# Optimization experiments

Measured on AMD Instinct MI355X. Metric: run time of the kernel, lower is better.

## Reference

```python
import jax, jax.numpy as jnp
import numpy as np

N, FIN, NH, NR, F, E = 50000, 256, 4, 4, 64, 500000


def setup_inputs() -> dict:
    key = jax.random.key(0)
    ks = jax.random.split(key, 12)
    x = jax.random.normal(ks[0], (N, FIN), jnp.float32)
    src = jax.random.randint(ks[1], (E,), 0, N)
    trg = jax.random.randint(ks[2], (E,), 0, N)
    rel = jax.random.randint(ks[3], (E,), 0, NR)
    node_to_graph_map = jnp.zeros((N,), jnp.int32)
    s = 1.0 / np.sqrt(FIN)
    W_proj = jax.random.uniform(ks[4], (NH * NR * F, FIN), jnp.float32, -s, s)
    score_src = jax.random.normal(ks[5], (1, NH, NR, F), jnp.float32) * 0.1
    score_trg = jax.random.normal(ks[6], (1, NH, NR, F), jnp.float32) * 0.1
    sf = 1.0 / np.sqrt(F)
    W1 = jax.random.uniform(ks[7], (F, F), jnp.float32, -sf, sf)
    b1 = jnp.zeros((F,), jnp.float32)
    W2 = jax.random.uniform(ks[8], (F, F), jnp.float32, -sf, sf)
    b2 = jnp.zeros((F,), jnp.float32)
    W3 = jax.random.uniform(ks[9], (1, F), jnp.float32, -sf, sf)
    b3 = jnp.zeros((1,), jnp.float32)
    W_skip = jax.random.uniform(ks[10], (NH * F, FIN), jnp.float32, -s, s)
    bias = jnp.zeros((NH * F,), jnp.float32)
    gamma = jnp.ones((NH * F,), jnp.float32)
    beta = jnp.zeros((NH * F,), jnp.float32)
    return dict(x=x, src=src, trg=trg, rel=rel, node_to_graph_map=node_to_graph_map,
                W_proj=W_proj, score_src=score_src, score_trg=score_trg,
                W1=W1, b1=b1, W2=W2, b2=b2, W3=W3, b3=b3,
                W_skip=W_skip, bias=bias, gamma=gamma, beta=beta)


def mish(v):
    return v * jnp.tanh(jax.nn.softplus(v))


def gat_forward(x, W_proj, score_src, score_trg, W1, b1, W2, b2, W3, b3,
                W_skip, bias, gamma, beta, src, trg, rel):
    n = x.shape[0]
    # (N, NH, NR, F) projected node features
    proj = (x @ W_proj.T).reshape(n, NH, NR, F)
    s_src = (proj * score_src).sum(-1)  # (N, NH, NR)
    s_trg = (proj * score_trg).sum(-1)  # (N, NH, NR)
    # lift to edges for their own relation: (E, NH)
    e_s = s_src[src, :, rel] + s_trg[trg, :, rel]
    e_s = jax.nn.leaky_relu(e_s, 0.2)
    # per-(relation, head) max over edges (matches per-relation max(dim=0) in the torch loop)
    m = jax.ops.segment_max(e_s, rel, num_segments=NR)  # (NR, NH)
    e_exp = jnp.exp(e_s - m[rel])
    # segment softmax grouped by (target node, relation)
    seg = trg * NR + rel
    denom = jax.ops.segment_sum(e_exp, seg, num_segments=n * NR)  # (N*NR, NH)
    att = e_exp / (denom[seg] + 1e-16)  # (E, NH)
    feat = proj[src, :, rel, :] * att[:, :, None]  # (E, NH, F)
    agg = jax.ops.segment_sum(feat, seg, num_segments=n * NR)  # (N*NR, NH, F)
    agg = agg.reshape(n, NR, NH, F).transpose(0, 2, 1, 3)  # (N, NH, NR, F)
    # AttentionedAggregationLayer: MLP score -> Mish -> softmax over relation dim -> weighted sum
    h = jax.nn.relu(agg @ W1.T + b1)
    h = jax.nn.relu(h @ W2.T + b2)
    sc = mish(h @ W3.T + b3)            # (N, NH, NR, 1)
    a_rel = jax.nn.softmax(sc, axis=-2)
    out = (agg * a_rel).sum(-2)          # (N, NH, F)
    # skip connection (FIN != NH*F per-head, so projected skip), concat heads, bias, ELU, LayerNorm
    out = out + (x @ W_skip.T).reshape(n, NH, F)
    out = out.reshape(n, NH * F) + bias
    out = jax.nn.elu(out)
    mu = out.mean(-1, keepdims=True)
    var = out.var(-1, keepdims=True)
    out = (out - mu) * jax.lax.rsqrt(var + 1e-5) * gamma + beta
    return out


def reference(x, src, trg, rel, node_to_graph_map, W_proj, score_src, score_trg,
              W1, b1, W2, b2, W3, b3, W_skip, bias, gamma, beta):
    return gat_forward(x, W_proj, score_src, score_trg, W1, b1, W2, b2, W3, b3,
                       W_skip, bias, gamma, beta, src, trg, rel)
```

## Files before the change

kernel.cpp:

```cpp
#include <hip/hip_runtime.h>

#define NNODES 50000
#define NEDGES 500000
#define NBINS  (NNODES * 4)
#define NSCANB 196
#define MPAD   50176

#define WF_W1    0
#define WF_B1    4096
#define WF_W2    4160
#define WF_B2    8256
#define WF_W3    8320
#define WF_B3    8384
#define WF_SSC   8388
#define WF_STC   9412
#define WF_BIAS  10436
#define WF_GAMMA 10692
#define WF_BETA  10948
#define WF_TOT   11204

typedef __attribute__((ext_vector_type(8))) short short8;
typedef __attribute__((ext_vector_type(4))) short short4v;
typedef __attribute__((ext_vector_type(4))) float floatx4;
typedef __attribute__((ext_vector_type(4))) unsigned int uint4v;

__device__ __forceinline__ float bf2f(unsigned short u) {
    return __uint_as_float(((unsigned)u) << 16);
}
__device__ __forceinline__ unsigned f2bf(float f) {
    unsigned u = __float_as_uint(f);
    u += 0x7fffu + ((u >> 16) & 1u);
    return u >> 16;
}
__device__ __forceinline__ int clampi(int v, int hi) { return v < 0 ? 0 : (v > hi ? hi : v); }

__device__ __forceinline__ short8 pack_bf16(const float* p) {
    short8 r;
#pragma unroll
    for (int j = 0; j < 8; j++) r[j] = (short)f2bf(p[j]);
    return r;
}

__global__ __launch_bounds__(256) void probe_k(const unsigned short* __restrict__ xs,
                                               unsigned* __restrict__ flag) {
    __shared__ unsigned cnt;
    if (threadIdx.x == 0) cnt = 0;
    __syncthreads();
    unsigned local = 0;
    for (int i = threadIdx.x; i < 8192; i += 256) {
        float v = bf2f(xs[i]);
        if (!(fabsf(v) < 1e10f)) local++;
    }
    atomicAdd(&cnt, local);
    __syncthreads();
    if (threadIdx.x == 0) *flag = (cnt > 256u) ? 1u : 0u;
}

__device__ __forceinline__ float ldf(const void* p, int i, bool f32) {
    return f32 ? ((const float*)p)[i] : bf2f(((const unsigned short*)p)[i]);
}

__global__ __launch_bounds__(1024) void wconv_k(const void* W1, const void* b1,
                                                const void* W2, const void* b2,
                                                const void* W3, const void* b3,
                                                const void* ssc, const void* stc,
                                                const void* bias, const void* gamma,
                                                const void* beta,
                                                const unsigned* __restrict__ flag,
                                                float* __restrict__ wf) {
    bool f32 = (*flag != 0u);
    for (int i = threadIdx.x; i < WF_TOT; i += 1024) {
        float v;
        if (i < WF_B1)          v = ldf(W1, i - WF_W1, f32);
        else if (i < WF_W2)     v = ldf(b1, i - WF_B1, f32);
        else if (i < WF_B2)     v = ldf(W2, i - WF_W2, f32);
        else if (i < WF_W3)     v = ldf(b2, i - WF_B2, f32);
        else if (i < WF_B3)     v = ldf(W3, i - WF_W3, f32);
        else if (i < WF_SSC) {
            int j = i - WF_B3;
            v = (j < 1) ? ldf(b3, j, f32) : 0.f;
        }
        else if (i < WF_STC)    v = ldf(ssc, i - WF_SSC, f32);
        else if (i < WF_BIAS)   v = ldf(stc, i - WF_STC, f32);
        else if (i < WF_GAMMA)  v = ldf(bias, i - WF_BIAS, f32);
        else if (i < WF_BETA)   v = ldf(gamma, i - WF_GAMMA, f32);
        else                    v = ldf(beta, i - WF_BETA, f32);
        wf[i] = v;
    }
}

__global__ __launch_bounds__(256) void convbf_k(const void* __restrict__ src,
                                                unsigned short* __restrict__ dst,
                                                int nelem, int npad,
                                                const unsigned* __restrict__ flag) {
    int i8 = (blockIdx.x * 256 + threadIdx.x) * 8;
    if (i8 >= npad) return;
    short8 o;
    if (i8 < nelem) {
        if (*flag) {
            const float* pf = (const float*)src + i8;
            floatx4 a = *(const floatx4*)pf;
            floatx4 b = *(const floatx4*)(pf + 4);
            o[0] = (short)f2bf(a[0]); o[1] = (short)f2bf(a[1]);
            o[2] = (short)f2bf(a[2]); o[3] = (short)f2bf(a[3]);
            o[4] = (short)f2bf(b[0]); o[5] = (short)f2bf(b[1]);
            o[6] = (short)f2bf(b[2]); o[7] = (short)f2bf(b[3]);
        } else {
            o = *(const short8*)((const unsigned short*)src + i8);
        }
    } else {
#pragma unroll
        for (int j = 0; j < 8; j++) o[j] = 0;
    }
    *(short8*)(dst + i8) = o;
}

__global__ __launch_bounds__(64) void gemm_fused_k(const unsigned short* __restrict__ A,
                                                   const unsigned short* __restrict__ Bp,
                                                   const unsigned short* __restrict__ Bs,
                                                   unsigned short* __restrict__ proj,
                                                   unsigned short* __restrict__ out16,
                                                   float* __restrict__ out32,
                                                   const float* __restrict__ wf,
                                                   float* __restrict__ s_src,
                                                   float* __restrict__ s_trg,
                                                   const unsigned* __restrict__ flag) {
    const bool cf32 = (*flag != 0u);
    const int lane = threadIdx.x & 63;
    const int l15 = lane & 15, q = lane >> 4;
    const int m0 = blockIdx.x * 64;
    const int cg0 = blockIdx.y * 4;

    short8 af[4][8];
#pragma unroll
    for (int mt = 0; mt < 4; mt++)
#pragma unroll
        for (int ks = 0; ks < 8; ks++)
            af[mt][ks] = *(const short8*)(A + (size_t)(m0 + mt * 16 + l15) * 256 + ks * 32 + q * 8);

    if (cg0 < 16) {
#pragma unroll 1
        for (int cgi = 0; cgi < 4; cgi++) {
            const int cg = cg0 + cgi;
            floatx4 acc[4][4];
#pragma unroll
            for (int i = 0; i < 4; i++)
#pragma unroll
                for (int j = 0; j < 4; j++) acc[i][j] = (floatx4){0.f, 0.f, 0.f, 0.f};
#pragma unroll
            for (int ks = 0; ks < 8; ks++) {
                short8 bfr[4];
#pragma unroll
                for (int nt = 0; nt < 4; nt++)
                    bfr[nt] = *(const short8*)(Bp + (size_t)(cg * 64 + nt * 16 + l15) * 256 + ks * 32 + q * 8);
#pragma unroll
                for (int mt = 0; mt < 4; mt++)
#pragma unroll
                    for (int nt = 0; nt < 4; nt++)
                        acc[mt][nt] = __builtin_amdgcn_mfma_f32_16x16x32_bf16(bfr[nt], af[mt][ks],
                                                                             acc[mt][nt], 0, 0, 0);
            }
            const int h = cg >> 2, r = cg & 3;
            const int colbase = (r * 4 + h) * 64;
            const int cell = r * 4 + h;
            const int scell = h * 4 + r;
            floatx4 sa4[4], sb4[4];
#pragma unroll
            for (int nt = 0; nt < 4; nt++) {
                sa4[nt] = *(const floatx4*)(wf + WF_SSC + scell * 64 + nt * 16 + q * 4);
                sb4[nt] = *(const floatx4*)(wf + WF_STC + scell * 64 + nt * 16 + q * 4);
            }
#pragma unroll
            for (int mt = 0; mt < 4; mt++) {
                const int row = m0 + mt * 16 + l15;
                float pa = 0.f, pb = 0.f;
#pragma unroll
                for (int nt = 0; nt < 4; nt++) {
                    short4v sv;
#pragma unroll
                    for (int rg = 0; rg < 4; rg++) {
                        float v = acc[mt][nt][rg];
                        unsigned short vb = (unsigned short)f2bf(v);
                        sv[rg] = (short)vb;
                        float vr = bf2f(vb);
                        pa = fmaf(vr, sa4[nt][rg], pa);
                        pb = fmaf(vr, sb4[nt][rg], pb);
                    }
                    if (row < NNODES)
                        *(short4v*)(proj + (size_t)row * 1024 + colbase + nt * 16 + q * 4) = sv;
                }
                pa += __shfl_xor(pa, 16);
                pa += __shfl_xor(pa, 32);
                pb += __shfl_xor(pb, 16);
                pb += __shfl_xor(pb, 32);
                if (q == 0 && row < NNODES) {
                    s_src[row * 16 + cell] = pa;
                    s_trg[row * 16 + cell] = pb;
                }
            }
        }
    } else {
#pragma unroll 1
        for (int cg = 0; cg < 4; cg++) {
            floatx4 acc[4][4];
#pragma unroll
            for (int i = 0; i < 4; i++)
#pragma unroll
                for (int j = 0; j < 4; j++) acc[i][j] = (floatx4){0.f, 0.f, 0.f, 0.f};
#pragma unroll
            for (int ks = 0; ks < 8; ks++) {
                short8 bfr[4];
#pragma unroll
                for (int nt = 0; nt < 4; nt++)
                    bfr[nt] = *(const short8*)(Bs + (size_t)(cg * 64 + nt * 16 + l15) * 256 + ks * 32 + q * 8);
#pragma unroll
                for (int mt = 0; mt < 4; mt++)
#pragma unroll
                    for (int nt = 0; nt < 4; nt++)
                        acc[mt][nt] = __builtin_amdgcn_mfma_f32_16x16x32_bf16(bfr[nt], af[mt][ks],
                                                                             acc[mt][nt], 0, 0, 0);
            }
#pragma unroll
            for (int mt = 0; mt < 4; mt++) {
                const int row = m0 + mt * 16 + l15;
                if (row >= NNODES) continue;
#pragma unroll
                for (int nt = 0; nt < 4; nt++) {
                    if (cf32) {
                        floatx4 o = acc[mt][nt];
                        *(floatx4*)(out32 + (size_t)row * 256 + cg * 64 + nt * 16 + q * 4) = o;
                    } else {
                        short4v sv;
#pragma unroll
                        for (int rg = 0; rg < 4; rg++)
                            sv[rg] = (short)f2bf(acc[mt][nt][rg]);
                        *(short4v*)(out16 + (size_t)row * 256 + cg * 64 + nt * 16 + q * 4) = sv;
                    }
                }
            }
        }
    }
}

__global__ __launch_bounds__(256) void count_k(const int* __restrict__ trg,
                                               const int* __restrict__ rel,
                                               unsigned* __restrict__ counts, int E) {
    int e = blockIdx.x * 256 + threadIdx.x;
    if (e >= E) return;
    int g = clampi(trg[e], NNODES - 1);
    int r = clampi(rel[e], 3);
    atomicAdd(&counts[g * 4 + r], 1u);
}

__global__ __launch_bounds__(256) void scan1_k(const unsigned* __restrict__ counts,
                                               unsigned* __restrict__ offsets,
                                               unsigned* __restrict__ bsum) {
    __shared__ unsigned ts[256];
    int t = threadIdx.x;
    int base = blockIdx.x * 1024 + t * 4;
    uint4v c = {0u, 0u, 0u, 0u};
    if (base + 3 < NBINS) c = *(const uint4v*)(counts + base);
    else {
#pragma unroll
        for (int j = 0; j < 4; j++) c[j] = (base + j < NBINS) ? counts[base + j] : 0u;
    }
    ts[t] = c[0] + c[1] + c[2] + c[3];
    __syncthreads();
    for (int off = 1; off < 256; off <<= 1) {
        unsigned v = (t >= off) ? ts[t - off] : 0u;
        __syncthreads();
        ts[t] += v;
        __syncthreads();
    }
    unsigned pre = (t == 0) ? 0u : ts[t - 1];
    uint4v o;
    o[0] = pre;
    o[1] = pre + c[0];
    o[2] = pre + c[0] + c[1];
    o[3] = pre + c[0] + c[1] + c[2];
    if (base + 3 < NBINS) *(uint4v*)(offsets + base) = o;
    else {
#pragma unroll
        for (int j = 0; j < 4; j++) if (base + j < NBINS) offsets[base + j] = o[j];
    }
    if (t == 255) bsum[blockIdx.x] = ts[255];
}

__global__ __launch_bounds__(256) void scan2_k(unsigned* __restrict__ bsum,
                                               unsigned* __restrict__ offsets) {
    __shared__ unsigned ts[256];
    int t = threadIdx.x;
    unsigned v = (t < NSCANB) ? bsum[t] : 0u;
    ts[t] = v;
    __syncthreads();
    for (int off = 1; off < 256; off <<= 1) {
        unsigned u = (t >= off) ? ts[t - off] : 0u;
        __syncthreads();
        ts[t] += u;
        __syncthreads();
    }
    if (t < NSCANB) bsum[t] = (t == 0) ? 0u : ts[t - 1];
    if (t == 255) offsets[NBINS] = ts[255];
}

__global__ __launch_bounds__(256) void scan3_k(unsigned* __restrict__ offsets,
                                               unsigned* __restrict__ cursor,
                                               const unsigned* __restrict__ bsum) {
    int t = threadIdx.x;
    unsigned base = bsum[blockIdx.x];
    int idx = blockIdx.x * 1024 + t * 4;
    if (idx + 3 < NBINS) {
        uint4v o = *(const uint4v*)(offsets + idx);
        o[0] += base; o[1] += base; o[2] += base; o[3] += base;
        *(uint4v*)(offsets + idx) = o;
        *(uint4v*)(cursor + idx) = o;
    } else {
#pragma unroll
        for (int j = 0; j < 4; j++)
            if (idx + j < NBINS) {
                unsigned v = offsets[idx + j] + base;
                offsets[idx + j] = v;
                cursor[idx + j] = v;
            }
    }
}

__global__ __launch_bounds__(256) void fill_k(const int* __restrict__ src,
                                              const int* __restrict__ trg,
                                              const int* __restrict__ rel,
                                              const float* __restrict__ s_src,
                                              const float* __restrict__ s_trg,
                                              unsigned* __restrict__ cursor,
                                              unsigned* __restrict__ esrc,
                                              floatx4* __restrict__ eexp, int E) {
    int e = blockIdx.x * 256 + threadIdx.x;
    if (e >= E) return;
    int s = clampi(src[e], NNODES - 1);
    int g = clampi(trg[e], NNODES - 1);
    int r = clampi(rel[e], 3);
    unsigned pos = atomicAdd(&cursor[g * 4 + r], 1u);
    if (pos >= (unsigned)E) pos = E - 1;
    esrc[pos] = (unsigned)s;
    floatx4 aa = *(const floatx4*)(s_src + s * 16 + r * 4);
    floatx4 bb = *(const floatx4*)(s_trg + g * 16 + r * 4);
    floatx4 v;
#pragma unroll
    for (int h = 0; h < 4; h++) {
        float val = aa[h] + bb[h];
        val = val > 0.f ? val : 0.2f * val;
        v[h] = expf(val);
    }
    eexp[pos] = v;
}

__global__ __launch_bounds__(256) void rowagg2_k(const unsigned* __restrict__ offsets,
                                                 const unsigned* __restrict__ esrc,
                                                 const floatx4* __restrict__ eexp,
                                                 const unsigned short* __restrict__ proj,
                                                 unsigned short* __restrict__ agg) {
    int wave = threadIdx.x >> 6, lane = threadIdx.x & 63;
    int bin = blockIdx.x * 4 + wave;
    if (bin >= NBINS) return;
    int r = bin & 3;
    int h = lane >> 4;
    unsigned beg = offsets[bin], end = offsets[bin + 1];

    float a0 = 0.f, a1 = 0.f, a2 = 0.f, a3 = 0.f, den = 0.f;
    unsigned i = beg;
    for (; i + 2 <= end; i += 2) {
        unsigned s0 = esrc[i], s1 = esrc[i + 1];
        floatx4 pe0 = eexp[i], pe1 = eexp[i + 1];
        short4v v0 = *((const short4v*)(proj + (size_t)s0 * 1024 + r * 256) + lane);
        short4v v1 = *((const short4v*)(proj + (size_t)s1 * 1024 + r * 256) + lane);
        float p0 = pe0[h], p1 = pe1[h];
        den += p0 + p1;
        a0 = fmaf(p0, bf2f((unsigned short)v0[0]), a0);
        a1 = fmaf(p0, bf2f((unsigned short)v0[1]), a1);
        a2 = fmaf(p0, bf2f((unsigned short)v0[2]), a2);
        a3 = fmaf(p0, bf2f((unsigned short)v0[3]), a3);
        a0 = fmaf(p1, bf2f((unsigned short)v1[0]), a0);
        a1 = fmaf(p1, bf2f((unsigned short)v1[1]), a1);
        a2 = fmaf(p1, bf2f((unsigned short)v1[2]), a2);
        a3 = fmaf(p1, bf2f((unsigned short)v1[3]), a3);
    }
    if (i < end) {
        unsigned s0 = esrc[i];
        floatx4 pe0 = eexp[i];
        short4v v0 = *((const short4v*)(proj + (size_t)s0 * 1024 + r * 256) + lane);
        float p0 = pe0[h];
        den += p0;
        a0 = fmaf(p0, bf2f((unsigned short)v0[0]), a0);
        a1 = fmaf(p0, bf2f((unsigned short)v0[1]), a1);
        a2 = fmaf(p0, bf2f((unsigned short)v0[2]), a2);
        a3 = fmaf(p0, bf2f((unsigned short)v0[3]), a3);
    }
    float inv = 1.f / (den + 1e-16f);
    short4v o;
    o[0] = (short)f2bf(a0 * inv);
    o[1] = (short)f2bf(a1 * inv);
    o[2] = (short)f2bf(a2 * inv);
    o[3] = (short)f2bf(a3 * inv);
    *((short4v*)(agg + (size_t)bin * 256) + lane) = o;
}

__global__ __launch_bounds__(256, 2) void mlp_mfma_k(const unsigned short* __restrict__ agg,
                                                     const float* __restrict__ wf,
                                                     float* __restrict__ sc) {
    __shared__ float lds[4][16 * 68];
    const int wave = threadIdx.x >> 6;
    const int lane = threadIdx.x & 63;
    const int l15 = lane & 15, q = lane >> 4;
    float* L = lds[wave];

    short8 w1f[2][4], w2f[2][4];
#pragma unroll
    for (int ks = 0; ks < 2; ks++)
#pragma unroll
        for (int nt = 0; nt < 4; nt++) {
            w1f[ks][nt] = pack_bf16(wf + WF_W1 + (nt * 16 + l15) * 64 + ks * 32 + q * 8);
            w2f[ks][nt] = pack_bf16(wf + WF_W2 + (nt * 16 + l15) * 64 + ks * 32 + q * 8);
        }
    float b1v[4], b2v[4], w3v[4];
#pragma unroll
    for (int nt = 0; nt < 4; nt++) {
        b1v[nt] = wf[WF_B1 + nt * 16 + l15];
        b2v[nt] = wf[WF_B2 + nt * 16 + l15];
        w3v[nt] = wf[WF_W3 + nt * 16 + l15];
    }
    float b3v = wf[WF_B3];

    int wave_id = blockIdx.x * 4 + wave;
#pragma unroll 1
    for (int t = 0; t < 4; t++) {
        int row0 = (wave_id * 4 + t) * 16;
        short8 a1[2];
#pragma unroll
        for (int ks = 0; ks < 2; ks++)
            a1[ks] = *(const short8*)(agg + (size_t)(row0 + l15) * 64 + ks * 32 + q * 8);
        floatx4 acc1[4];
#pragma unroll
        for (int nt = 0; nt < 4; nt++) {
            acc1[nt] = (floatx4){0.f, 0.f, 0.f, 0.f};
            acc1[nt] = __builtin_amdgcn_mfma_f32_16x16x32_bf16(a1[0], w1f[0][nt], acc1[nt], 0, 0, 0);
            acc1[nt] = __builtin_amdgcn_mfma_f32_16x16x32_bf16(a1[1], w1f[1][nt], acc1[nt], 0, 0, 0);
        }
#pragma unroll
        for (int nt = 0; nt < 4; nt++)
#pragma unroll
            for (int rg = 0; rg < 4; rg++)
                L[(q * 4 + rg) * 68 + nt * 16 + l15] = fmaxf(acc1[nt][rg] + b1v[nt], 0.f);
        short8 a2[2];
#pragma unroll
        for (int ks = 0; ks < 2; ks++) {
            short8 rr;
#pragma unroll
            for (int j = 0; j < 8; j++)
                rr[j] = (short)f2bf(L[l15 * 68 + ks * 32 + q * 8 + j]);
            a2[ks] = rr;
        }
        floatx4 acc2[4];
#pragma unroll
        for (int nt = 0; nt < 4; nt++) {
            acc2[nt] = (floatx4){0.f, 0.f, 0.f, 0.f};
            acc2[nt] = __builtin_amdgcn_mfma_f32_16x16x32_bf16(a2[0], w2f[0][nt], acc2[nt], 0, 0, 0);
            acc2[nt] = __builtin_amdgcn_mfma_f32_16x16x32_bf16(a2[1], w2f[1][nt], acc2[nt], 0, 0, 0);
        }
        float p[4];
#pragma unroll
        for (int rg = 0; rg < 4; rg++) {
            float s = 0.f;
#pragma unroll
            for (int nt = 0; nt < 4; nt++)
                s = fmaf(fmaxf(acc2[nt][rg] + b2v[nt], 0.f), w3v[nt], s);
            p[rg] = s;
        }
#pragma unroll
        for (int off = 1; off < 16; off <<= 1) {
#pragma unroll
            for (int rg = 0; rg < 4; rg++) p[rg] += __shfl_xor(p[rg], off);
        }
        if (l15 == 0) {
#pragma unroll
            for (int rg = 0; rg < 4; rg++) {
                float acc = p[rg] + b3v;
                float sp = fmaxf(acc, 0.f) + log1pf(expf(-fabsf(acc)));
                float m = acc * tanhf(sp);
                int s_id = row0 + q * 4 + rg;
                int n = s_id >> 4, r = (s_id >> 2) & 3, h = s_id & 3;
                sc[n * 16 + h * 4 + r] = m;
            }
        }
    }
}

__global__ __launch_bounds__(256) void final_k(const unsigned short* __restrict__ agg,
                                               const float* __restrict__ sc,
                                               const float* __restrict__ wf,
                                               const unsigned* __restrict__ flag,
                                               unsigned short* __restrict__ out16,
                                               float* __restrict__ out32) {
    const bool f32 = (*flag != 0u);
    const int wave = threadIdx.x >> 6, lane = threadIdx.x & 63;
    const int n = blockIdx.x * 4 + wave;
    const int h = lane >> 4;
    const int c0 = h * 64 + (lane & 15) * 4;

    floatx4 sv = *(const floatx4*)(sc + n * 16 + h * 4);
    float mx = fmaxf(fmaxf(sv[0], sv[1]), fmaxf(sv[2], sv[3]));
    float e0 = expf(sv[0] - mx), e1 = expf(sv[1] - mx);
    float e2 = expf(sv[2] - mx), e3 = expf(sv[3] - mx);
    float inv = 1.f / (e0 + e1 + e2 + e3);
    float er[4] = {e0 * inv, e1 * inv, e2 * inv, e3 * inv};

    float acc4[4] = {0.f, 0.f, 0.f, 0.f};
#pragma unroll
    for (int r = 0; r < 4; r++) {
        short4v av = *(const short4v*)(agg + (size_t)n * 1024 + r * 256 + c0);
        float e = er[r];
        acc4[0] = fmaf(e, bf2f((unsigned short)av[0]), acc4[0]);
        acc4[1] = fmaf(e, bf2f((unsigned short)av[1]), acc4[1]);
        acc4[2] = fmaf(e, bf2f((unsigned short)av[2]), acc4[2]);
        acc4[3] = fmaf(e, bf2f((unsigned short)av[3]), acc4[3]);
    }

    const size_t ob = (size_t)n * 256 + c0;
    float v[4];
    floatx4 bi = *(const floatx4*)(wf + WF_BIAS + c0);
    if (f32) {
        floatx4 sk = *(const floatx4*)(out32 + ob);
#pragma unroll
        for (int j = 0; j < 4; j++) v[j] = acc4[j] + sk[j] + bi[j];
    } else {
        short4v sk = *(const short4v*)(out16 + ob);
#pragma unroll
        for (int j = 0; j < 4; j++) v[j] = acc4[j] + bf2f((unsigned short)sk[j]) + bi[j];
    }
#pragma unroll
    for (int j = 0; j < 4; j++) v[j] = v[j] > 0.f ? v[j] : expm1f(v[j]);

    float s = v[0] + v[1] + v[2] + v[3];
    float qq = v[0] * v[0] + v[1] * v[1] + v[2] * v[2] + v[3] * v[3];
#pragma unroll
    for (int o = 1; o < 64; o <<= 1) {
        s += __shfl_xor(s, o);
        qq += __shfl_xor(qq, o);
    }
    float mu = s * (1.f / 256.f);
    float var = fmaxf(qq * (1.f / 256.f) - mu * mu, 0.f);
    float rstd = rsqrtf(var + 1e-5f);

    floatx4 ga = *(const floatx4*)(wf + WF_GAMMA + c0);
    floatx4 be = *(const floatx4*)(wf + WF_BETA + c0);
    if (f32) {
        floatx4 o4;
#pragma unroll
        for (int j = 0; j < 4; j++) o4[j] = (v[j] - mu) * rstd * ga[j] + be[j];
        *(floatx4*)(out32 + ob) = o4;
    } else {
        short4v o4;
#pragma unroll
        for (int j = 0; j < 4; j++) o4[j] = (short)f2bf((v[j] - mu) * rstd * ga[j] + be[j]);
        *(short4v*)(out16 + ob) = o4;
    }
}

extern "C" void kernel_launch(void* const* d_in, const int* in_sizes, int n_in,
                              void* d_out, int out_size, void* d_ws, size_t ws_size,
                              hipStream_t stream) {
    if (ws_size < 226900000) return;

    const void* x      = d_in[0];
    const int* src     = (const int*)d_in[1];
    const int* trg     = (const int*)d_in[2];
    const int* rel     = (const int*)d_in[3];
    const void* W_proj = d_in[5];
    const void* ssc    = d_in[6];
    const void* stc    = d_in[7];
    const void* W1     = d_in[8];
    const void* b1     = d_in[9];
    const void* W2     = d_in[10];
    const void* b2     = d_in[11];
    const void* W3     = d_in[12];
    const void* b3     = d_in[13];
    const void* W_skip = d_in[14];
    const void* bias   = d_in[15];
    const void* gamma  = d_in[16];
    const void* beta   = d_in[17];
    unsigned short* out16 = (unsigned short*)d_out;
    float* out32          = (float*)d_out;

    char* w = (char*)d_ws;
    unsigned short* proj = (unsigned short*)(w + 0);
    unsigned short* agg  = (unsigned short*)(w + 102400000);
    unsigned short* xbf  = (unsigned short*)(w + 102400000);
    float* s_src         = (float*)(w + 204800000);
    float* s_trg         = (float*)(w + 208000000);
    floatx4* eexp        = (floatx4*)(w + 211200000);
    unsigned short* wpbf = (unsigned short*)(w + 211200000);
    unsigned short* wsbf = (unsigned short*)(w + 212300000);
    unsigned* esrc       = (unsigned*)(w + 219200000);
    unsigned* counts     = (unsigned*)(w + 221200000);
    unsigned* offsets    = (unsigned*)(w + 222000000);
    unsigned* cursor     = (unsigned*)(w + 222800016);
    float* sc            = (float*)(w + 223600016);
    float* wf            = (float*)(w + 226800016);
    unsigned* flag       = (unsigned*)(w + 226844840);
    unsigned* bsum       = (unsigned*)(w + 226844848);

    hipMemsetAsync(counts, 0, NBINS * 4, stream);

    probe_k<<<1, 256, 0, stream>>>((const unsigned short*)x, flag);
    wconv_k<<<1, 1024, 0, stream>>>(W1, b1, W2, b2, W3, b3, ssc, stc, bias, gamma, beta,
                                    flag, wf);
    convbf_k<<<(MPAD * 256) / (8 * 256), 256, 0, stream>>>(x, xbf, NNODES * 256,
                                                           MPAD * 256, flag);
    convbf_k<<<128, 256, 0, stream>>>(W_proj, wpbf, 1024 * 256, 1024 * 256, flag);
    convbf_k<<<32, 256, 0, stream>>>(W_skip, wsbf, 256 * 256, 256 * 256, flag);
    gemm_fused_k<<<dim3(784, 5), 64, 0, stream>>>(xbf, wpbf, wsbf, proj, out16, out32,
                                                  wf, s_src, s_trg, flag);
    count_k<<<1954, 256, 0, stream>>>(trg, rel, counts, NEDGES);
    scan1_k<<<NSCANB, 256, 0, stream>>>(counts, offsets, bsum);
    scan2_k<<<1, 256, 0, stream>>>(bsum, offsets);
    scan3_k<<<NSCANB, 256, 0, stream>>>(offsets, cursor, bsum);
    fill_k<<<1954, 256, 0, stream>>>(src, trg, rel, s_src, s_trg, cursor, esrc, eexp, NEDGES);
    rowagg2_k<<<NBINS / 4, 256, 0, stream>>>(offsets, esrc, eexp, proj, agg);
    mlp_mfma_k<<<3125, 256, 0, stream>>>(agg, wf, sc);
    final_k<<<12500, 256, 0, stream>>>(agg, sc, wf, flag, out16, out32);
}
```

Measured before the change: 532.8 us.

## Fuse edge aggregation, relation MLP and final LayerNorm into one per-node kernel

Merges the row aggregation, MFMA MLP scoring and final softmax/skip/ELU/LayerNorm kernels into one kernel. Each wave handles whole nodes and keeps the aggregated features in LDS, so the agg and score buffers never go through global memory. MLP weights are converted to bf16 once in the weight conversion kernel instead of in every wave. The cost is fewer independent waves for the irregular gather (3125 blocks, each wave walking 4 nodes serially) and more LDS per block, which may reduce latency hiding for the gather.

```diff
diff --git a/kernel.cpp b/kernel.cpp
--- a/kernel.cpp
+++ b/kernel.cpp
@@ -18,6 +18,7 @@
 #define WF_GAMMA 10692
 #define WF_BETA  10948
 #define WF_TOT   11204
+#define WB_TOT   8192
 
 typedef __attribute__((ext_vector_type(8))) short short8;
 typedef __attribute__((ext_vector_type(4))) short short4v;
@@ -33,13 +34,6 @@
     return u >> 16;
 }
 __device__ __forceinline__ int clampi(int v, int hi) { return v < 0 ? 0 : (v > hi ? hi : v); }
-
-__device__ __forceinline__ short8 pack_bf16(const float* p) {
-    short8 r;
-#pragma unroll
-    for (int j = 0; j < 8; j++) r[j] = (short)f2bf(p[j]);
-    return r;
-}
 
 __global__ __launch_bounds__(256) void probe_k(const unsigned short* __restrict__ xs,
                                                unsigned* __restrict__ flag) {
@@ -67,9 +61,16 @@
                                                 const void* bias, const void* gamma,
                                                 const void* beta,
                                                 const unsigned* __restrict__ flag,
-                                                float* __restrict__ wf) {
+                                                float* __restrict__ wf,
+                                                unsigned short* __restrict__ wbf16) {
     bool f32 = (*flag != 0u);
-    for (int i = threadIdx.x; i < WF_TOT; i += 1024) {
+    for (int i = threadIdx.x; i < WF_TOT + WB_TOT; i += 1024) {
+        if (i >= WF_TOT) {
+            int j = i - WF_TOT;
+            float v = (j < 4096) ? ldf(W1, j, f32) : ldf(W2, j - 4096, f32);
+            wbf16[j] = (unsigned short)f2bf(v);
+            continue;
+        }
         float v;
         if (i < WF_B1)          v = ldf(W1, i - WF_W1, f32);
         else if (i < WF_W2)     v = ldf(b1, i - WF_B1, f32);
@@ -353,19 +354,10 @@
     eexp[pos] = v;
 }
 
-__global__ __launch_bounds__(256) void rowagg2_k(const unsigned* __restrict__ offsets,
-                                                 const unsigned* __restrict__ esrc,
-                                                 const floatx4* __restrict__ eexp,
-                                                 const unsigned short* __restrict__ proj,
-                                                 unsigned short* __restrict__ agg) {
-    int wave = threadIdx.x >> 6, lane = threadIdx.x & 63;
-    int bin = blockIdx.x * 4 + wave;
-    if (bin >= NBINS) return;
-    int r = bin & 3;
-    int h = lane >> 4;
-    unsigned beg = offsets[bin], end = offsets[bin + 1];
-
-    float a0 = 0.f, a1 = 0.f, a2 = 0.f, a3 = 0.f, den = 0.f;
+__device__ __forceinline__ void edge_acc(const unsigned* esrc, const floatx4* eexp,
+                                         const unsigned short* proj, int r, int h,
+                                         int lane, unsigned beg, unsigned end,
+                                         float* a, float* den) {
     unsigned i = beg;
     for (; i + 2 <= end; i += 2) {
         unsigned s0 = esrc[i], s1 = esrc[i + 1];
@@ -373,52 +365,54 @@
         short4v v0 = *((const short4v*)(proj + (size_t)s0 * 1024 + r * 256) + lane);
         short4v v1 = *((const short4v*)(proj + (size_t)s1 * 1024 + r * 256) + lane);
         float p0 = pe0[h], p1 = pe1[h];
-        den += p0 + p1;
-        a0 = fmaf(p0, bf2f((unsigned short)v0[0]), a0);
-        a1 = fmaf(p0, bf2f((unsigned short)v0[1]), a1);
-        a2 = fmaf(p0, bf2f((unsigned short)v0[2]), a2);
-        a3 = fmaf(p0, bf2f((unsigned short)v0[3]), a3);
-        a0 = fmaf(p1, bf2f((unsigned short)v1[0]), a0);
-        a1 = fmaf(p1, bf2f((unsigned short)v1[1]), a1);
-        a2 = fmaf(p1, bf2f((unsigned short)v1[2]), a2);
-        a3 = fmaf(p1, bf2f((unsigned short)v1[3]), a3);
+        *den += p0 + p1;
+        a[0] = fmaf(p0, bf2f((unsigned short)v0[0]), a[0]);
+        a[1] = fmaf(p0, bf2f((unsigned short)v0[1]), a[1]);
+        a[2] = fmaf(p0, bf2f((unsigned short)v0[2]), a[2]);
+        a[3] = fmaf(p0, bf2f((unsigned short)v0[3]), a[3]);
+        a[0] = fmaf(p1, bf2f((unsigned short)v1[0]), a[0]);
+        a[1] = fmaf(p1, bf2f((unsigned short)v1[1]), a[1]);
+        a[2] = fmaf(p1, bf2f((unsigned short)v1[2]), a[2]);
+        a[3] = fmaf(p1, bf2f((unsigned short)v1[3]), a[3]);
     }
     if (i < end) {
         unsigned s0 = esrc[i];
         floatx4 pe0 = eexp[i];
         short4v v0 = *((const short4v*)(proj + (size_t)s0 * 1024 + r * 256) + lane);
         float p0 = pe0[h];
-        den += p0;
-        a0 = fmaf(p0, bf2f((unsigned short)v0[0]), a0);
-        a1 = fmaf(p0, bf2f((unsigned short)v0[1]), a1);
-        a2 = fmaf(p0, bf2f((unsigned short)v0[2]), a2);
-        a3 = fmaf(p0, bf2f((unsigned short)v0[3]), a3);
-    }
-    float inv = 1.f / (den + 1e-16f);
-    short4v o;
-    o[0] = (short)f2bf(a0 * inv);
-    o[1] = (short)f2bf(a1 * inv);
-    o[2] = (short)f2bf(a2 * inv);
-    o[3] = (short)f2bf(a3 * inv);
-    *((short4v*)(agg + (size_t)bin * 256) + lane) = o;
-}
-
-__global__ __launch_bounds__(256, 2) void mlp_mfma_k(const unsigned short* __restrict__ agg,
-                                                     const float* __restrict__ wf,
-                                                     float* __restrict__ sc) {
-    __shared__ float lds[4][16 * 68];
+        *den += p0;
+        a[0] = fmaf(p0, bf2f((unsigned short)v0[0]), a[0]);
+        a[1] = fmaf(p0, bf2f((unsigned short)v0[1]), a[1]);
+        a[2] = fmaf(p0, bf2f((unsigned short)v0[2]), a[2]);
+        a[3] = fmaf(p0, bf2f((unsigned short)v0[3]), a[3]);
+    }
+}
+
+__global__ __launch_bounds__(256) void node_fused_k(const unsigned* __restrict__ offsets,
+                                                    const unsigned* __restrict__ esrc,
+                                                    const floatx4* __restrict__ eexp,
+                                                    const unsigned short* __restrict__ proj,
+                                                    const unsigned short* __restrict__ wbf16,
+                                                    const float* __restrict__ wf,
+                                                    const unsigned* __restrict__ flag,
+                                                    unsigned short* __restrict__ out16,
+                                                    float* __restrict__ out32) {
+    __shared__ unsigned short aggL[4][16 * 72];
+    __shared__ float hidL[4][16 * 68];
+    const bool f32 = (*flag != 0u);
     const int wave = threadIdx.x >> 6;
     const int lane = threadIdx.x & 63;
     const int l15 = lane & 15, q = lane >> 4;
-    float* L = lds[wave];
+    unsigned short* aL = aggL[wave];
+    float* hL = hidL[wave];
 
     short8 w1f[2][4], w2f[2][4];
 #pragma unroll
     for (int ks = 0; ks < 2; ks++)
 #pragma unroll
         for (int nt = 0; nt < 4; nt++) {
-            w1f[ks][nt] = pack_bf16(wf + WF_W1 + (nt * 16 + l15) * 64 + ks * 32 + q * 8);
-            w2f[ks][nt] = pack_bf16(wf + WF_W2 + (nt * 16 + l15) * 64 + ks * 32 + q * 8);
+            w1f[ks][nt] = *(const short8*)(wbf16 + (nt * 16 + l15) * 64 + ks * 32 + q * 8);
+            w2f[ks][nt] = *(const short8*)(wbf16 + 4096 + (nt * 16 + l15) * 64 + ks * 32 + q * 8);
         }
     float b1v[4], b2v[4], w3v[4];
 #pragma unroll
@@ -427,16 +421,38 @@
         b2v[nt] = wf[WF_B2 + nt * 16 + l15];
         w3v[nt] = wf[WF_W3 + nt * 16 + l15];
     }
-    float b3v = wf[WF_B3];
-
-    int wave_id = blockIdx.x * 4 + wave;
+    const float b3v = wf[WF_B3];
+
+    const int c0 = q * 64 + l15 * 4;
+    const floatx4 bi = *(const floatx4*)(wf + WF_BIAS + c0);
+    const floatx4 ga = *(const floatx4*)(wf + WF_GAMMA + c0);
+    const floatx4 be = *(const floatx4*)(wf + WF_BETA + c0);
+
+    const int wave_id = blockIdx.x * 4 + wave;
 #pragma unroll 1
     for (int t = 0; t < 4; t++) {
-        int row0 = (wave_id * 4 + t) * 16;
+        const int n = wave_id * 4 + t;
+
+#pragma unroll
+        for (int r = 0; r < 4; r++) {
+            const int bin = n * 4 + r;
+            unsigned beg = offsets[bin], end = offsets[bin + 1];
+            float a[4] = {0.f, 0.f, 0.f, 0.f};
+            float den = 0.f;
+            edge_acc(esrc, eexp, proj, r, q, lane, beg, end, a, &den);
+            float inv = 1.f / (den + 1e-16f);
+            short4v o;
+            o[0] = (short)f2bf(a[0] * inv);
+            o[1] = (short)f2bf(a[1] * inv);
+            o[2] = (short)f2bf(a[2] * inv);
+            o[3] = (short)f2bf(a[3] * inv);
+            *(short4v*)(aL + (r * 4 + q) * 72 + l15 * 4) = o;
+        }
+
         short8 a1[2];
 #pragma unroll
         for (int ks = 0; ks < 2; ks++)
-            a1[ks] = *(const short8*)(agg + (size_t)(row0 + l15) * 64 + ks * 32 + q * 8);
+            a1[ks] = *(const short8*)(aL + l15 * 72 + ks * 32 + q * 8);
         floatx4 acc1[4];
 #pragma unroll
         for (int nt = 0; nt < 4; nt++) {
@@ -448,14 +464,14 @@
         for (int nt = 0; nt < 4; nt++)
 #pragma unroll
             for (int rg = 0; rg < 4; rg++)
-                L[(q * 4 + rg) * 68 + nt * 16 + l15] = fmaxf(acc1[nt][rg] + b1v[nt], 0.f);
+                hL[(q * 4 + rg) * 68 + nt * 16 + l15] = fmaxf(acc1[nt][rg] + b1v[nt], 0.f);
         short8 a2[2];
 #pragma unroll
         for (int ks = 0; ks < 2; ks++) {
             short8 rr;
 #pragma unroll
             for (int j = 0; j < 8; j++)
-                rr[j] = (short)f2bf(L[l15 * 68 + ks * 32 + q * 8 + j]);
+                rr[j] = (short)f2bf(hL[l15 * 68 + ks * 32 + q * 8 + j]);
             a2[ks] = rr;
         }
         floatx4 acc2[4];
@@ -479,88 +495,69 @@
 #pragma unroll
             for (int rg = 0; rg < 4; rg++) p[rg] += __shfl_xor(p[rg], off);
         }
-        if (l15 == 0) {
-#pragma unroll
-            for (int rg = 0; rg < 4; rg++) {
-                float acc = p[rg] + b3v;
-                float sp = fmaxf(acc, 0.f) + log1pf(expf(-fabsf(acc)));
-                float m = acc * tanhf(sp);
-                int s_id = row0 + q * 4 + rg;
-                int n = s_id >> 4, r = (s_id >> 2) & 3, h = s_id & 3;
-                sc[n * 16 + h * 4 + r] = m;
-            }
-        }
-    }
-}
-
-__global__ __launch_bounds__(256) void final_k(const unsigned short* __restrict__ agg,
-                                               const float* __restrict__ sc,
-                                               const float* __restrict__ wf,
-                                               const unsigned* __restrict__ flag,
-                                               unsigned short* __restrict__ out16,
-                                               float* __restrict__ out32) {
-    const bool f32 = (*flag != 0u);
-    const int wave = threadIdx.x >> 6, lane = threadIdx.x & 63;
-    const int n = blockIdx.x * 4 + wave;
-    const int h = lane >> 4;
-    const int c0 = h * 64 + (lane & 15) * 4;
-
-    floatx4 sv = *(const floatx4*)(sc + n * 16 + h * 4);
-    float mx = fmaxf(fmaxf(sv[0], sv[1]), fmaxf(sv[2], sv[3]));
-    float e0 = expf(sv[0] - mx), e1 = expf(sv[1] - mx);
-    float e2 = expf(sv[2] - mx), e3 = expf(sv[3] - mx);
-    float inv = 1.f / (e0 + e1 + e2 + e3);
-    float er[4] = {e0 * inv, e1 * inv, e2 * inv, e3 * inv};
-
-    float acc4[4] = {0.f, 0.f, 0.f, 0.f};
-#pragma unroll
-    for (int r = 0; r < 4; r++) {
-        short4v av = *(const short4v*)(agg + (size_t)n * 1024 + r * 256 + c0);
-        float e = er[r];
-        acc4[0] = fmaf(e, bf2f((unsigned short)av[0]), acc4[0]);
-        acc4[1] = fmaf(e, bf2f((unsigned short)av[1]), acc4[1]);
-        acc4[2] = fmaf(e, bf2f((unsigned short)av[2]), acc4[2]);
-        acc4[3] = fmaf(e, bf2f((unsigned short)av[3]), acc4[3]);
-    }
-
-    const size_t ob = (size_t)n * 256 + c0;
-    float v[4];
-    floatx4 bi = *(const floatx4*)(wf + WF_BIAS + c0);
-    if (f32) {
-        floatx4 sk = *(const floatx4*)(out32 + ob);
-#pragma unroll
-        for (int j = 0; j < 4; j++) v[j] = acc4[j] + sk[j] + bi[j];
-    } else {
-        short4v sk = *(const short4v*)(out16 + ob);
-#pragma unroll
-        for (int j = 0; j < 4; j++) v[j] = acc4[j] + bf2f((unsigned short)sk[j]) + bi[j];
-    }
-#pragma unroll
-    for (int j = 0; j < 4; j++) v[j] = v[j] > 0.f ? v[j] : expm1f(v[j]);
-
-    float s = v[0] + v[1] + v[2] + v[3];
-    float qq = v[0] * v[0] + v[1] * v[1] + v[2] * v[2] + v[3] * v[3];
-#pragma unroll
-    for (int o = 1; o < 64; o <<= 1) {
-        s += __shfl_xor(s, o);
-        qq += __shfl_xor(qq, o);
-    }
-    float mu = s * (1.f / 256.f);
-    float var = fmaxf(qq * (1.f / 256.f) - mu * mu, 0.f);
-    float rstd = rsqrtf(var + 1e-5f);
-
-    floatx4 ga = *(const floatx4*)(wf + WF_GAMMA + c0);
-    floatx4 be = *(const floatx4*)(wf + WF_BETA + c0);
-    if (f32) {
-        floatx4 o4;
-#pragma unroll
-        for (int j = 0; j < 4; j++) o4[j] = (v[j] - mu) * rstd * ga[j] + be[j];
-        *(floatx4*)(out32 + ob) = o4;
-    } else {
-        short4v o4;
-#pragma unroll
-        for (int j = 0; j < 4; j++) o4[j] = (short)f2bf((v[j] - mu) * rstd * ga[j] + be[j]);
-        *(short4v*)(out16 + ob) = o4;
+        float psel = (l15 & 2) ? ((l15 & 1) ? p[3] : p[2])
+                               : ((l15 & 1) ? p[1] : p[0]);
+        float acc = psel + b3v;
+        float sp = fmaxf(acc, 0.f) + log1pf(expf(-fabsf(acc)));
+        float msh = acc * tanhf(sp);
+
+        float sv0 = __shfl(msh, 0 * 16 + q);
+        float sv1 = __shfl(msh, 1 * 16 + q);
+        float sv2 = __shfl(msh, 2 * 16 + q);
+        float sv3 = __shfl(msh, 3 * 16 + q);
+        float mx = fmaxf(fmaxf(sv0, sv1), fmaxf(sv2, sv3));
+        float e0 = expf(sv0 - mx), e1 = expf(sv1 - mx);
+        float e2 = expf(sv2 - mx), e3 = expf(sv3 - mx);
+        float inv = 1.f / (e0 + e1 + e2 + e3);
+        float er[4] = {e0 * inv, e1 * inv, e2 * inv, e3 * inv};
+
+        float acc4[4] = {0.f, 0.f, 0.f, 0.f};
+#pragma unroll
+        for (int r = 0; r < 4; r++) {
+            short4v av = *(const short4v*)(aL + (r * 4 + q) * 72 + l15 * 4);
+            float e = er[r];
+            acc4[0] = fmaf(e, bf2f((unsigned short)av[0]), acc4[0]);
+            acc4[1] = fmaf(e, bf2f((unsigned short)av[1]), acc4[1]);
+            acc4[2] = fmaf(e, bf2f((unsigned short)av[2]), acc4[2]);
+            acc4[3] = fmaf(e, bf2f((unsigned short)av[3]), acc4[3]);
+        }
+
+        const size_t ob = (size_t)n * 256 + c0;
+        float v[4];
+        if (f32) {
+            floatx4 sk = *(const floatx4*)(out32 + ob);
+#pragma unroll
+            for (int j = 0; j < 4; j++) v[j] = acc4[j] + sk[j] + bi[j];
+        } else {
+            short4v sk = *(const short4v*)(out16 + ob);
+#pragma unroll
+            for (int j = 0; j < 4; j++) v[j] = acc4[j] + bf2f((unsigned short)sk[j]) + bi[j];
+        }
+#pragma unroll
+        for (int j = 0; j < 4; j++) v[j] = v[j] > 0.f ? v[j] : expm1f(v[j]);
+
+        float s = v[0] + v[1] + v[2] + v[3];
+        float qq = v[0] * v[0] + v[1] * v[1] + v[2] * v[2] + v[3] * v[3];
+#pragma unroll
+        for (int o = 1; o < 64; o <<= 1) {
+            s += __shfl_xor(s, o);
+            qq += __shfl_xor(qq, o);
+        }
+        float mu = s * (1.f / 256.f);
+        float var = fmaxf(qq * (1.f / 256.f) - mu * mu, 0.f);
+        float rstd = rsqrtf(var + 1e-5f);
+
+        if (f32) {
+            floatx4 o4;
+#pragma unroll
+            for (int j = 0; j < 4; j++) o4[j] = (v[j] - mu) * rstd * ga[j] + be[j];
+            *(floatx4*)(out32 + ob) = o4;
+        } else {
+            short4v o4;
+#pragma unroll
+            for (int j = 0; j < 4; j++) o4[j] = (short)f2bf((v[j] - mu) * rstd * ga[j] + be[j]);
+            *(short4v*)(out16 + ob) = o4;
+        }
     }
 }
 
@@ -591,7 +588,6 @@
 
     char* w = (char*)d_ws;
     unsigned short* proj = (unsigned short*)(w + 0);
-    unsigned short* agg  = (unsigned short*)(w + 102400000);
     unsigned short* xbf  = (unsigned short*)(w + 102400000);
     float* s_src         = (float*)(w + 204800000);
     float* s_trg         = (float*)(w + 208000000);
@@ -602,16 +598,16 @@
     unsigned* counts     = (unsigned*)(w + 221200000);
     unsigned* offsets    = (unsigned*)(w + 222000000);
     unsigned* cursor     = (unsigned*)(w + 222800016);
-    float* sc            = (float*)(w + 223600016);
     float* wf            = (float*)(w + 226800016);
-    unsigned* flag       = (unsigned*)(w + 226844840);
-    unsigned* bsum       = (unsigned*)(w + 226844848);
+    unsigned short* wbf16= (unsigned short*)(w + 226844832);
+    unsigned* flag       = (unsigned*)(w + 226861216);
+    unsigned* bsum       = (unsigned*)(w + 226861224);
 
     hipMemsetAsync(counts, 0, NBINS * 4, stream);
 
     probe_k<<<1, 256, 0, stream>>>((const unsigned short*)x, flag);
     wconv_k<<<1, 1024, 0, stream>>>(W1, b1, W2, b2, W3, b3, ssc, stc, bias, gamma, beta,
-                                    flag, wf);
+                                    flag, wf, wbf16);
     convbf_k<<<(MPAD * 256) / (8 * 256), 256, 0, stream>>>(x, xbf, NNODES * 256,
                                                            MPAD * 256, flag);
     convbf_k<<<128, 256, 0, stream>>>(W_proj, wpbf, 1024 * 256, 1024 * 256, flag);
@@ -623,7 +619,6 @@
     scan2_k<<<1, 256, 0, stream>>>(bsum, offsets);
     scan3_k<<<NSCANB, 256, 0, stream>>>(offsets, cursor, bsum);
     fill_k<<<1954, 256, 0, stream>>>(src, trg, rel, s_src, s_trg, cursor, esrc, eexp, NEDGES);
-    rowagg2_k<<<NBINS / 4, 256, 0, stream>>>(offsets, esrc, eexp, proj, agg);
-    mlp_mfma_k<<<3125, 256, 0, stream>>>(agg, wf, sc);
-    final_k<<<12500, 256, 0, stream>>>(agg, sc, wf, flag, out16, out32);
-}
+    node_fused_k<<<3125, 256, 0, stream>>>(offsets, esrc, eexp, proj, wbf16, wf, flag,
+                                           out16, out32);
+}
```

After: 509.0 us. 1.05x faster.
